# Kernel optimization log

Measured on AMD Instinct MI355X. Metric: run time of the kernel, lower is better.

Reference implementation:

```python
import jax, jax.numpy as jnp
import numpy as np

IMG_SHAPE = (256, 256, 256)


def _rot3(a):
    # Rx @ Ry @ Rz, matching _compute_rotation
    ax, ay, az = a[0], a[1], a[2]
    cx, sx = jnp.cos(ax), jnp.sin(ax)
    cy, sy = jnp.cos(ay), jnp.sin(ay)
    cz, sz = jnp.cos(az), jnp.sin(az)
    one = jnp.ones_like(ax)
    zero = jnp.zeros_like(ax)
    Rx = jnp.stack([jnp.stack([one, zero, zero]),
                    jnp.stack([zero, cx, -sx]),
                    jnp.stack([zero, sx, cx])])
    Ry = jnp.stack([jnp.stack([cy, zero, sy]),
                    jnp.stack([zero, one, zero]),
                    jnp.stack([-sy, zero, cy])])
    Rz = jnp.stack([jnp.stack([cz, -sz, zero]),
                    jnp.stack([sz, cz, zero]),
                    jnp.stack([zero, zero, one])])
    return Rx @ Ry @ Rz


def _rigid4(a, t, cog):
    # T_center_inv @ T_trans @ T_rot @ T_center
    R = _rot3(a)
    Tc = jnp.eye(4, dtype=a.dtype).at[:3, 3].set(-cog)
    Tci = jnp.eye(4, dtype=a.dtype).at[:3, 3].set(cog)
    Tt = jnp.eye(4, dtype=a.dtype).at[:3, 3].set(t)
    Tr = jnp.eye(4, dtype=a.dtype).at[:3, :3].set(R)
    return Tci @ Tt @ Tr @ Tc


def _trilinear(vol, di, dj, dk):
    # fast_3D_interp_torch(mode='linear'): trilinear interp, zero outside bounds
    D, H, W = vol.shape
    ok = (di >= 0) & (di <= D - 1) & (dj >= 0) & (dj <= H - 1) & (dk >= 0) & (dk <= W - 1)
    di = jnp.clip(di, 0.0, D - 1)
    dj = jnp.clip(dj, 0.0, H - 1)
    dk = jnp.clip(dk, 0.0, W - 1)
    fi = jnp.floor(di).astype(jnp.int32)
    fj = jnp.floor(dj).astype(jnp.int32)
    fk = jnp.floor(dk).astype(jnp.int32)
    ci = jnp.clip(fi + 1, 0, D - 1)
    cj = jnp.clip(fj + 1, 0, H - 1)
    ck = jnp.clip(fk + 1, 0, W - 1)
    wi = di - fi
    wj = dj - fj
    wk = dk - fk
    out = (vol[fi, fj, fk] * (1 - wi) * (1 - wj) * (1 - wk)
           + vol[fi, fj, ck] * (1 - wi) * (1 - wj) * wk
           + vol[fi, cj, fk] * (1 - wi) * wj * (1 - wk)
           + vol[fi, cj, ck] * (1 - wi) * wj * wk
           + vol[ci, fj, fk] * wi * (1 - wj) * (1 - wk)
           + vol[ci, fj, ck] * wi * (1 - wj) * wk
           + vol[ci, cj, fk] * wi * wj * (1 - wk)
           + vol[ci, cj, ck] * wi * wj * wk)
    return jnp.where(ok, out, jnp.zeros_like(out))


def setup_inputs() -> dict:
    key = jax.random.key(0)
    k1, k2 = jax.random.split(key)
    image_targ = jax.random.normal(k1, (1, 1) + IMG_SHAPE, dtype=jnp.float32)
    # small rotation so most of the warped grid stays in bounds (angle_factor=1)
    angle = 0.1 * jax.random.normal(k2, (1, 3), dtype=jnp.float32)
    translation = jnp.zeros((1, 3), dtype=jnp.float32)
    v2r = np.eye(4, dtype=np.float32)
    v2r[:3, 3] = -127.5  # center-of-volume RAS origin
    ref_v2r = jnp.asarray(v2r)
    flo_v2r = jnp.asarray(v2r)
    cog = jnp.zeros((3,), dtype=jnp.float32)
    return {"image_targ": image_targ, "angle": angle, "translation": translation,
            "ref_v2r": ref_v2r, "flo_v2r": flo_v2r, "cog": cog}


def reference(image_targ, angle, translation, ref_v2r, flo_v2r, cog):
    # tx_factor = angle_factor = 1 -> params used as-is
    T_rig = jax.vmap(lambda a, t: _rigid4(a, t, cog))(angle, translation)  # [B,4,4]
    T = (jnp.linalg.inv(flo_v2r) @ T_rig[0] @ ref_v2r).astype(jnp.float32)
    D, H, W = image_targ.shape[2:]
    gi, gj, gk = jnp.meshgrid(jnp.arange(D, dtype=jnp.float32),
                              jnp.arange(H, dtype=jnp.float32),
                              jnp.arange(W, dtype=jnp.float32), indexing='ij')
    di = T[0, 0] * gi + T[0, 1] * gj + T[0, 2] * gk + T[0, 3]
    dj = T[1, 0] * gi + T[1, 1] * gj + T[1, 2] * gk + T[1, 3]
    dk = T[2, 0] * gi + T[2, 1] * gj + T[2, 2] * gk + T[2, 3]
    image_reg = _trilinear(image_targ[0, 0], di, dj, dk)
    return image_reg[None, None]
```

## Files before the change

kernel.cpp:

```cpp
#include <hip/hip_runtime.h>
#include <math.h>

#define DD 256
#define HH 256
#define WW 256
#define IPT 4

typedef float f2v __attribute__((ext_vector_type(2)));
typedef f2v __attribute__((aligned(4))) f2u;

__global__ void compute_T_kernel(const float* __restrict__ angle,
                                 const float* __restrict__ trans,
                                 const float* __restrict__ ref_v2r,
                                 const float* __restrict__ flo_v2r,
                                 const float* __restrict__ cog,
                                 float* __restrict__ Tout ) {
    if (blockIdx.x != 0 || threadIdx.x != 0) return;

    const float ax = angle[0], ay = angle[1], az = angle[2];
    const float cx = cosf(ax), sx = sinf(ax);
    const float cy = cosf(ay), sy = sinf(ay);
    const float cz = cosf(az), sz = sinf(az);

    float R[3][3];
    const float a00 = cy,       a01 = 0.0f, a02 = sy;
    const float a10 = sx * sy,  a11 = cx,   a12 = -sx * cy;
    const float a20 = -cx * sy, a21 = sx,   a22 = cx * cy;
    R[0][0] = a00 * cz + a01 * sz; R[0][1] = -a00 * sz + a01 * cz; R[0][2] = a02;
    R[1][0] = a10 * cz + a11 * sz; R[1][1] = -a10 * sz + a11 * cz; R[1][2] = a12;
    R[2][0] = a20 * cz + a21 * sz; R[2][1] = -a20 * sz + a21 * cz; R[2][2] = a22;

    float Trig[4][4];
    for (int r = 0; r < 4; ++r)
        for (int c = 0; c < 4; ++c)
            Trig[r][c] = (r == c) ? 1.0f : 0.0f;
    for (int r = 0; r < 3; ++r) {
        for (int c = 0; c < 3; ++c) Trig[r][c] = R[r][c];
        Trig[r][3] = cog[r] + trans[r]
                   - (R[r][0] * cog[0] + R[r][1] * cog[1] + R[r][2] * cog[2]);
    }

    float m[16], inv[16];
    for (int q = 0; q < 16; ++q) m[q] = flo_v2r[q];
    inv[0]  =  m[5]*m[10]*m[15] - m[5]*m[11]*m[14] - m[9]*m[6]*m[15]
             + m[9]*m[7]*m[14] + m[13]*m[6]*m[11] - m[13]*m[7]*m[10];
    inv[4]  = -m[4]*m[10]*m[15] + m[4]*m[11]*m[14] + m[8]*m[6]*m[15]
             - m[8]*m[7]*m[14] - m[12]*m[6]*m[11] + m[12]*m[7]*m[10];
    inv[8]  =  m[4]*m[9]*m[15] - m[4]*m[11]*m[13] - m[8]*m[5]*m[15]
             + m[8]*m[7]*m[13] + m[12]*m[5]*m[11] - m[12]*m[7]*m[9];
    inv[12] = -m[4]*m[9]*m[14] + m[4]*m[10]*m[13] + m[8]*m[5]*m[14]
             - m[8]*m[6]*m[13] - m[12]*m[5]*m[10] + m[12]*m[6]*m[9];
    inv[1]  = -m[1]*m[10]*m[15] + m[1]*m[11]*m[14] + m[9]*m[2]*m[15]
             - m[9]*m[3]*m[14] - m[13]*m[2]*m[11] + m[13]*m[3]*m[10];
    inv[5]  =  m[0]*m[10]*m[15] - m[0]*m[11]*m[14] - m[8]*m[2]*m[15]
             + m[8]*m[3]*m[14] + m[12]*m[2]*m[11] - m[12]*m[3]*m[10];
    inv[9]  = -m[0]*m[9]*m[15] + m[0]*m[11]*m[13] + m[8]*m[1]*m[15]
             - m[8]*m[3]*m[13] - m[12]*m[1]*m[11] + m[12]*m[3]*m[9];
    inv[13] =  m[0]*m[9]*m[14] - m[0]*m[10]*m[13] - m[8]*m[1]*m[14]
             + m[8]*m[2]*m[13] + m[12]*m[1]*m[10] - m[12]*m[2]*m[9];
    inv[2]  =  m[1]*m[6]*m[15] - m[1]*m[7]*m[14] - m[5]*m[2]*m[15]
             + m[5]*m[3]*m[14] + m[13]*m[2]*m[7] - m[13]*m[3]*m[6];
    inv[6]  = -m[0]*m[6]*m[15] + m[0]*m[7]*m[14] + m[4]*m[2]*m[15]
             - m[4]*m[3]*m[14] - m[12]*m[2]*m[7] + m[12]*m[3]*m[6];
    inv[10] =  m[0]*m[5]*m[15] - m[0]*m[7]*m[13] - m[4]*m[1]*m[15]
             + m[4]*m[3]*m[13] + m[12]*m[1]*m[7] - m[12]*m[3]*m[5];
    inv[14] = -m[0]*m[5]*m[14] + m[0]*m[6]*m[13] + m[4]*m[1]*m[14]
             - m[4]*m[2]*m[13] - m[12]*m[1]*m[6] + m[12]*m[2]*m[5];
    inv[3]  = -m[1]*m[6]*m[11] + m[1]*m[7]*m[10] + m[5]*m[2]*m[11]
             - m[5]*m[3]*m[10] - m[9]*m[2]*m[7] + m[9]*m[3]*m[6];
    inv[7]  =  m[0]*m[6]*m[11] - m[0]*m[7]*m[10] - m[4]*m[2]*m[11]
             + m[4]*m[3]*m[10] + m[8]*m[2]*m[7] - m[8]*m[3]*m[6];
    inv[11] = -m[0]*m[5]*m[11] + m[0]*m[7]*m[9] + m[4]*m[1]*m[11]
             - m[4]*m[3]*m[9] - m[8]*m[1]*m[7] + m[8]*m[3]*m[5];
    inv[15] =  m[0]*m[5]*m[10] - m[0]*m[6]*m[9] - m[4]*m[1]*m[10]
             + m[4]*m[2]*m[9] + m[8]*m[1]*m[6] - m[8]*m[2]*m[5];
    const float det = m[0]*inv[0] + m[1]*inv[4] + m[2]*inv[8] + m[3]*inv[12];
    const float rdet = 1.0f / det;

    float M1[4][4];
    for (int r = 0; r < 4; ++r)
        for (int c = 0; c < 4; ++c) {
            float s = 0.0f;
            for (int q = 0; q < 4; ++q) s += Trig[r][q] * ref_v2r[q * 4 + c];
            M1[r][c] = s;
        }
    for (int r = 0; r < 3; ++r)
        for (int c = 0; c < 4; ++c) {
            float s = 0.0f;
            for (int q = 0; q < 4; ++q) s += (inv[r * 4 + q] * rdet) * M1[q][c];
            Tout[r * 4 + c] = s;
        }
}

__global__ __launch_bounds__(256, 8) void warp_kernel(
        const float* __restrict__ vol,
        const float* __restrict__ T,
        float* __restrict__ out) {
    const float t0 = T[0],  t1 = T[1],  t2  = T[2],  t3  = T[3];
    const float t4 = T[4],  t5 = T[5],  t6  = T[6],  t7  = T[7];
    const float t8 = T[8],  t9 = T[9],  t10 = T[10], t11 = T[11];

    const int bid = blockIdx.x;
    const int xcd = bid & 7;
    const int n = bid >> 3;
    const int bi = (xcd >> 2) & 1;
    const int bj = (xcd >> 1) & 1;
    const int bk = xcd & 1;
    const int kt = n & 1;
    const int jt = (n >> 1) & 31;
    const int it = n >> 6;

    const int tx = threadIdx.x & 63;
    const int ty = threadIdx.x >> 6;

    const int i0 = (bi << 7) + it * IPT;
    const int j  = (bj << 7) + (jt << 2) + ty;
    const int k  = (bk << 7) + (kt << 6) + tx;

    const float gj = (float)j, gk = (float)k;
    const float di0 = t0 * (float)i0 + t1 * gj + t2  * gk + t3;
    const float dj0 = t4 * (float)i0 + t5 * gj + t6  * gk + t7;
    const float dk0 = t8 * (float)i0 + t9 * gj + t10 * gk + t11;

    f2v vv[IPT][4];
    float wv[IPT][3];
    {
        float di = di0, dj = dj0, dk = dk0;
#pragma unroll
        for (int s = 0; s < IPT; ++s) {
            const float cdi = fminf(fmaxf(di, 0.0f), (float)(DD - 1));
            const float cdj = fminf(fmaxf(dj, 0.0f), (float)(HH - 1));
            const float cdk = fminf(fmaxf(dk, 0.0f), (float)(WW - 1));

            const int fi = (int)cdi;
            const int fj = (int)cdj;
            const int fk = (int)cdk;
            const int ci = min(fi + 1, DD - 1);
            const int cj = min(fj + 1, HH - 1);
            const int pk = min(fk, WW - 2);

            wv[s][0] = cdi - (float)fi;
            wv[s][1] = cdj - (float)fj;
            wv[s][2] = cdk - (float)pk;

            const int fi_o = fi << 16, ci_o = ci << 16;
            const int fj_o = fj << 8,  cj_o = cj << 8;

            vv[s][0] = *(const f2u*)(vol + (fi_o + fj_o + pk));
            vv[s][1] = *(const f2u*)(vol + (fi_o + cj_o + pk));
            vv[s][2] = *(const f2u*)(vol + (ci_o + fj_o + pk));
            vv[s][3] = *(const f2u*)(vol + (ci_o + cj_o + pk));

            di += t0; dj += t4; dk += t8;
        }
    }

    __builtin_amdgcn_sched_barrier(0);
#pragma unroll
    for (int s = 0; s < IPT; ++s) {
#pragma unroll
        for (int c = 0; c < 4; ++c) {
            asm volatile("" : "+v"(vv[s][c]));
        }
    }
    __builtin_amdgcn_sched_barrier(0);

    const int out_base = (i0 << 16) + (j << 8) + k;
    {
        float di = di0, dj = dj0, dk = dk0;
#pragma unroll
        for (int s = 0; s < IPT; ++s) {
            const bool ok = (di >= 0.0f) & (di <= (float)(DD - 1)) &
                            (dj >= 0.0f) & (dj <= (float)(HH - 1)) &
                            (dk >= 0.0f) & (dk <= (float)(WW - 1));

            const float wi = wv[s][0];
            const float wj = wv[s][1];
            const float wk = wv[s][2];

            const float c00 = vv[s][0].x + (vv[s][0].y - vv[s][0].x) * wk;
            const float c01 = vv[s][1].x + (vv[s][1].y - vv[s][1].x) * wk;
            const float c10 = vv[s][2].x + (vv[s][2].y - vv[s][2].x) * wk;
            const float c11 = vv[s][3].x + (vv[s][3].y - vv[s][3].x) * wk;
            const float c0  = c00 + (c01 - c00) * wj;
            const float c1  = c10 + (c11 - c10) * wj;
            const float val = c0 + (c1 - c0) * wi;

            __builtin_nontemporal_store(ok ? val : 0.0f,
                                        &out[out_base + (s << 16)]);

            di += t0; dj += t4; dk += t8;
        }
    }
}

extern "C" void kernel_launch(void* const* d_in, const int* in_sizes, int n_in,
                              void* d_out, int out_size, void* d_ws, size_t ws_size,
                              hipStream_t stream) {
    const float* image_targ  = (const float*)d_in[0];
    const float* angle       = (const float*)d_in[1];
    const float* translation = (const float*)d_in[2];
    const float* ref_v2r     = (const float*)d_in[3];
    const float* flo_v2r     = (const float*)d_in[4];
    const float* cog         = (const float*)d_in[5];
    float* out = (float*)d_out;
    float* Tws = (float*)d_ws;

    compute_T_kernel<<<1, 64, 0, stream>>>(angle, translation, ref_v2r,
                                           flo_v2r, cog, Tws);
    warp_kernel<<<(DD * HH) / IPT, 256, 0, stream>>>(image_targ, Tws, out);
}
```

Baseline: 187.8 us.

## Software-pipeline the gather loads with double buffering over more i-slices per thread

Each thread now handles 32 i-slices in 8 groups of 4 instead of a single group of 4. Loads for the next group are issued into a second register buffer while the current group is interpolated and stored, so gather latency overlaps with math and stores inside one thread. The grid shrinks to 2048 blocks, which amortizes setup work, and the launch-bound occupancy hint drops from 8 to 4 to leave room for the extra registers. The trade-off is fewer resident waves to hide memory latency and less block-level parallelism.

```diff
diff --git a/kernel.cpp b/kernel.cpp
--- a/kernel.cpp
+++ b/kernel.cpp
@@ -4,7 +4,8 @@
 #define DD 256
 #define HH 256
 #define WW 256
-#define IPT 4
+#define G     4
+#define NITER 8
 
 typedef float f2v __attribute__((ext_vector_type(2)));
 typedef f2v __attribute__((aligned(4))) f2u;
@@ -92,7 +93,7 @@
         }
 }
 
-__global__ __launch_bounds__(256, 8) void warp_kernel(
+__global__ __launch_bounds__(256, 4) void warp_kernel(
         const float* __restrict__ vol,
         const float* __restrict__ T,
         float* __restrict__ out) {
@@ -108,90 +109,99 @@
     const int bk = xcd & 1;
     const int kt = n & 1;
     const int jt = (n >> 1) & 31;
-    const int it = n >> 6;
+    const int it2 = n >> 6;
 
     const int tx = threadIdx.x & 63;
     const int ty = threadIdx.x >> 6;
 
-    const int i0 = (bi << 7) + it * IPT;
+    const int i0 = (bi << 7) + (it2 << 5);
     const int j  = (bj << 7) + (jt << 2) + ty;
     const int k  = (bk << 7) + (kt << 6) + tx;
 
     const float gj = (float)j, gk = (float)k;
-    const float di0 = t0 * (float)i0 + t1 * gj + t2  * gk + t3;
-    const float dj0 = t4 * (float)i0 + t5 * gj + t6  * gk + t7;
-    const float dk0 = t8 * (float)i0 + t9 * gj + t10 * gk + t11;
-
-    f2v vv[IPT][4];
-    float wv[IPT][3];
-    {
-        float di = di0, dj = dj0, dk = dk0;
+    const int out_base = (i0 << 16) + (j << 8) + k;
+
+    f2v vA[G][4], vB[G][4];
+    float wA[G][3], wB[G][3];
+    unsigned int mA, mB;
+
+#define ISSUE(V, W, M, IT) do {                                              \
+    const float gi_ = (float)(i0 + (IT) * G);                                \
+    float di_ = t0 * gi_ + t1 * gj + t2  * gk + t3;                          \
+    float dj_ = t4 * gi_ + t5 * gj + t6  * gk + t7;                          \
+    float dk_ = t8 * gi_ + t9 * gj + t10 * gk + t11;                         \
+    M = 0u;                                                                  \
+    _Pragma("unroll")                                                        \
+    for (int s_ = 0; s_ < G; ++s_) {                                         \
+        const float cdi = fminf(fmaxf(di_, 0.0f), (float)(DD - 1));          \
+        const float cdj = fminf(fmaxf(dj_, 0.0f), (float)(HH - 1));          \
+        const float cdk = fminf(fmaxf(dk_, 0.0f), (float)(WW - 1));          \
+        const int fi = (int)cdi;                                             \
+        const int fj = (int)cdj;                                             \
+        const int fk = (int)cdk;                                             \
+        const int ci = min(fi + 1, DD - 1);                                  \
+        const int cj = min(fj + 1, HH - 1);                                  \
+        const int pk = min(fk, WW - 2);           \
+          \
+        W[s_][0] = cdi - (float)fi;                                          \
+        W[s_][1] = cdj - (float)fj;                                          \
+        W[s_][2] = cdk - (float)pk;                                          \
+        const bool ok_ = (di_ >= 0.0f) & (di_ <= (float)(DD - 1)) &          \
+                         (dj_ >= 0.0f) & (dj_ <= (float)(HH - 1)) &          \
+                         (dk_ >= 0.0f) & (dk_ <= (float)(WW - 1));           \
+        M |= (ok_ ? 1u : 0u) << s_;                                          \
+        const int fi_o = fi << 16, ci_o = ci << 16;                          \
+        const int fj_o = fj << 8,  cj_o = cj << 8;                           \
+        V[s_][0] = *(const f2u*)(vol + (fi_o + fj_o + pk));                  \
+        V[s_][1] = *(const f2u*)(vol + (fi_o + cj_o + pk));                  \
+        V[s_][2] = *(const f2u*)(vol + (ci_o + fj_o + pk));                  \
+        V[s_][3] = *(const f2u*)(vol + (ci_o + cj_o + pk));                  \
+        di_ += t0; dj_ += t4; dk_ += t8;                                     \
+    }                                                                        \
+} while (0)
+
+#define PIN(V) do {                                                          \
+    __builtin_amdgcn_sched_barrier(0);                                       \
+    _Pragma("unroll")                                                        \
+    for (int s_ = 0; s_ < G; ++s_) {                                         \
+        _Pragma("unroll")                                                    \
+        for (int c_ = 0; c_ < 4; ++c_) asm volatile("" : "+v"(V[s_][c_]));   \
+    }                                                                        \
+    __builtin_amdgcn_sched_barrier(0);                                       \
+} while (0)
+
+#define CONSUME(V, W, M, IT) do {                                            \
+    _Pragma("unroll")                                                        \
+    for (int s_ = 0; s_ < G; ++s_) {                                         \
+        const float wi = W[s_][0], wj = W[s_][1], wk = W[s_][2];             \
+        const float c00 = V[s_][0].x + (V[s_][0].y - V[s_][0].x) * wk;       \
+        const float c01 = V[s_][1].x + (V[s_][1].y - V[s_][1].x) * wk;       \
+        const float c10 = V[s_][2].x + (V[s_][2].y - V[s_][2].x) * wk;       \
+        const float c11 = V[s_][3].x + (V[s_][3].y - V[s_][3].x) * wk;       \
+        const float c0  = c00 + (c01 - c00) * wj;                            \
+        const float c1  = c10 + (c11 - c10) * wj;                            \
+        const float val = c0 + (c1 - c0) * wi;                               \
+        const bool ok_ = (M >> s_) & 1u;                                     \
+        __builtin_nontemporal_store(ok_ ? val : 0.0f,                        \
+            &out[out_base + ((((IT) * G) + s_) << 16)]);                     \
+    }                                                                        \
+} while (0)
+
+    ISSUE(vA, wA, mA, 0);
+
 #pragma unroll
-        for (int s = 0; s < IPT; ++s) {
-            const float cdi = fminf(fmaxf(di, 0.0f), (float)(DD - 1));
-            const float cdj = fminf(fmaxf(dj, 0.0f), (float)(HH - 1));
-            const float cdk = fminf(fmaxf(dk, 0.0f), (float)(WW - 1));
-
-            const int fi = (int)cdi;
-            const int fj = (int)cdj;
-            const int fk = (int)cdk;
-            const int ci = min(fi + 1, DD - 1);
-            const int cj = min(fj + 1, HH - 1);
-            const int pk = min(fk, WW - 2);
-
-            wv[s][0] = cdi - (float)fi;
-            wv[s][1] = cdj - (float)fj;
-            wv[s][2] = cdk - (float)pk;
-
-            const int fi_o = fi << 16, ci_o = ci << 16;
-            const int fj_o = fj << 8,  cj_o = cj << 8;
-
-            vv[s][0] = *(const f2u*)(vol + (fi_o + fj_o + pk));
-            vv[s][1] = *(const f2u*)(vol + (fi_o + cj_o + pk));
-            vv[s][2] = *(const f2u*)(vol + (ci_o + fj_o + pk));
-            vv[s][3] = *(const f2u*)(vol + (ci_o + cj_o + pk));
-
-            di += t0; dj += t4; dk += t8;
-        }
+    for (int ot = 0; ot < NITER / 2; ++ot) {
+        ISSUE(vB, wB, mB, 2 * ot + 1);
+        PIN(vA);
+        CONSUME(vA, wA, mA, 2 * ot);
+        if (2 * ot + 2 < NITER) ISSUE(vA, wA, mA, 2 * ot + 2);
+        PIN(vB);
+        CONSUME(vB, wB, mB, 2 * ot + 1);
     }
 
-    __builtin_amdgcn_sched_barrier(0);
-#pragma unroll
-    for (int s = 0; s < IPT; ++s) {
-#pragma unroll
-        for (int c = 0; c < 4; ++c) {
-            asm volatile("" : "+v"(vv[s][c]));
-        }
-    }
-    __builtin_amdgcn_sched_barrier(0);
-
-    const int out_base = (i0 << 16) + (j << 8) + k;
-    {
-        float di = di0, dj = dj0, dk = dk0;
-#pragma unroll
-        for (int s = 0; s < IPT; ++s) {
-            const bool ok = (di >= 0.0f) & (di <= (float)(DD - 1)) &
-                            (dj >= 0.0f) & (dj <= (float)(HH - 1)) &
-                            (dk >= 0.0f) & (dk <= (float)(WW - 1));
-
-            const float wi = wv[s][0];
-            const float wj = wv[s][1];
-            const float wk = wv[s][2];
-
-            const float c00 = vv[s][0].x + (vv[s][0].y - vv[s][0].x) * wk;
-            const float c01 = vv[s][1].x + (vv[s][1].y - vv[s][1].x) * wk;
-            const float c10 = vv[s][2].x + (vv[s][2].y - vv[s][2].x) * wk;
-            const float c11 = vv[s][3].x + (vv[s][3].y - vv[s][3].x) * wk;
-            const float c0  = c00 + (c01 - c00) * wj;
-            const float c1  = c10 + (c11 - c10) * wj;
-            const float val = c0 + (c1 - c0) * wi;
-
-            __builtin_nontemporal_store(ok ? val : 0.0f,
-                                        &out[out_base + (s << 16)]);
-
-            di += t0; dj += t4; dk += t8;
-        }
-    }
+#undef ISSUE
+#undef PIN
+#undef CONSUME
 }
 
 extern "C" void kernel_launch(void* const* d_in, const int* in_sizes, int n_in,
@@ -208,5 +218,6 @@
 
     compute_T_kernel<<<1, 64, 0, stream>>>(angle, translation, ref_v2r,
                                            flo_v2r, cog, Tws);
-    warp_kernel<<<(DD * HH) / IPT, 256, 0, stream>>>(image_targ, Tws, out);
+    warp_kernel<<<(DD * HH * WW) / (256 * G * NITER), 256, 0, stream>>>(
+        image_targ, Tws, out);
 }
```

After: 386.9 us. +106.0%, slower.
